# Optimization experiments

Hardware: AMD Instinct MI355X
Metric: run time of the kernel (lower is better)

## Reference

```python
import jax, jax.numpy as jnp
import numpy as np

GROUP_SIZE = 64  # quantization group size along in_features
RANK = 16
ALPHA = 1.0


def setup_inputs() -> dict:
    key = jax.random.key(0)
    ks = jax.random.split(key, 7)
    B, S, D_in, D_out = 4, 2048, 4096, 4096
    n_groups = D_in // GROUP_SIZE
    x = jax.random.normal(ks[0], (B, S, D_in), dtype=jnp.float32)
    qweight = jax.random.randint(ks[1], (D_out, D_in), 0, 16, dtype=jnp.int32)
    scales = jax.random.uniform(ks[2], (D_out, n_groups), dtype=jnp.float32) * 0.02
    zeros = jax.random.uniform(ks[3], (D_out, n_groups), dtype=jnp.float32) * 16.0
    lora_A = jax.random.normal(ks[4], (RANK, D_in), dtype=jnp.float32) / np.sqrt(D_in)
    lora_B = jax.random.normal(ks[5], (D_out, RANK), dtype=jnp.float32) * 0.01
    bias = jax.random.normal(ks[6], (D_out,), dtype=jnp.float32) * 0.02
    return {"x": x, "qweight": qweight, "scales": scales, "zeros": zeros,
            "lora_A": lora_A, "lora_B": lora_B, "bias": bias}


def _dequant(qweight, scales, zeros):
    # qweight: [O, I] int codes in [0,16); scales/zeros: [O, G] with G = I // GROUP_SIZE
    O, I = qweight.shape
    G = I // GROUP_SIZE
    q = qweight.astype(scales.dtype).reshape(O, G, GROUP_SIZE)
    w = (q - zeros[:, :, None]) * scales[:, :, None]
    return w.reshape(O, I)


def reference(x, qweight, scales, zeros, lora_A, lora_B, bias):
    # Base 4-bit dequantized matmul: y = x @ W^T
    W = _dequant(qweight, scales, zeros)            # [O, I]
    y = jnp.einsum('bsi,oi->bso', x, W)             # [B, S, O]
    # LoRA low-rank update: (alpha / rank) * (x @ A^T) @ B^T
    scaling = ALPHA / RANK
    lora = jnp.einsum('bsr,or->bso', jnp.einsum('bsi,ri->bsr', x, lora_A), lora_B)
    return y + scaling * lora + bias
```

## Files before the change

### kernel.cpp

```cpp
#include <hip/hip_runtime.h>
#include <stdint.h>
#include <stddef.h>

#define GM 8192
#define GN 4096
#define GK 4096
#define NGRP 64

typedef __bf16 bf16;
typedef __attribute__((ext_vector_type(8))) __bf16 bf16x8;
typedef __attribute__((ext_vector_type(4))) __bf16 bf16x4;
typedef __attribute__((ext_vector_type(4))) float floatx4;
typedef __attribute__((ext_vector_type(4))) int   intx4;
typedef __attribute__((ext_vector_type(8))) unsigned short ushortx8;
typedef __attribute__((ext_vector_type(4))) unsigned short ushortx4;

__device__ inline unsigned short f2bf(float f) {
  unsigned int u = __builtin_bit_cast(unsigned int, f);
  u += 0x7FFFu + ((u >> 16) & 1u);
  return (unsigned short)(u >> 16);
}
__device__ inline bf16x8 pack8(floatx4 a, floatx4 b) {
  ushortx8 u;
  u[0]=f2bf(a[0]); u[1]=f2bf(a[1]); u[2]=f2bf(a[2]); u[3]=f2bf(a[3]);
  u[4]=f2bf(b[0]); u[5]=f2bf(b[1]); u[6]=f2bf(b[2]); u[7]=f2bf(b[3]);
  return __builtin_bit_cast(bf16x8, u);
}
__device__ inline bf16x4 pack4(floatx4 a) {
  ushortx4 u;
  u[0]=f2bf(a[0]); u[1]=f2bf(a[1]); u[2]=f2bf(a[2]); u[3]=f2bf(a[3]);
  return __builtin_bit_cast(bf16x4, u);
}
__device__ inline void gll16(const void* g, void* l) {
  __builtin_amdgcn_global_load_lds(
      (const __attribute__((address_space(1))) void*)g,
      (__attribute__((address_space(3))) void*)l, 16, 0, 0);
}

__global__ __launch_bounds__(256) void qlora_prep(
    const float* __restrict__ x, bf16* __restrict__ xbf,
    const int* __restrict__ qw, const float* __restrict__ scales,
    const float* __restrict__ zeros, const float* __restrict__ lA,
    const float* __restrict__ lB, bf16* __restrict__ wbf) {
  __shared__ __align__(16) float Al[16 * 256];
  __shared__ __align__(16) float Bl[32 * 16];
  const int tid = threadIdx.x;

  if (blockIdx.x >= 2048) {
    int xb = blockIdx.x - 2048;
    #pragma unroll
    for (int t = 0; t < 4; ++t) {
      int fc = xb * 1024 + t * 256 + tid;
      int m  = fc >> 9;
      int rc = fc & 511;
      int p  = (rc & 7) ^ (m & 7);
      const float* src = x + ((size_t)fc << 3);
      floatx4 a = *(const floatx4*)src;
      floatx4 b = *(const floatx4*)(src + 4);
      *(bf16x8*)(xbf + (size_t)m * GK + ((rc >> 3) << 6) + (p << 3)) = pack8(a, b);
    }
    return;
  }

  const int n0  = (blockIdx.x & 127) * 32;
  const int kc0 = (blockIdx.x >> 7) * 256;
  #pragma unroll
  for (int t = 0; t < 4; ++t) {
    int idx = tid + t * 256;
    int r = idx >> 6, c = idx & 63;
    *(floatx4*)&Al[r * 256 + c * 4] = *(const floatx4*)&lA[(size_t)r * GK + kc0 + c * 4];
  }
  if (tid < 128) {
    int r = tid >> 2, c = tid & 3;
    *(floatx4*)&Bl[r * 16 + c * 4] = *(const floatx4*)&lB[(size_t)(n0 + r) * 16 + c * 4];
  }
  __syncthreads();

  const int klane = tid & 63;
  const int wv    = tid >> 6;
  const int k  = klane * 4;
  const int kg = kc0 + k;
  const int kb = kg & ~63;
  const int g  = kg >> 6;
  for (int it = 0; it < 8; ++it) {
    int nl = wv * 8 + it;
    int n  = n0 + nl;
    float Bv[16];
    #pragma unroll
    for (int r = 0; r < 16; ++r) Bv[r] = Bl[nl * 16 + r];
    floatx4 lacc = {0.f, 0.f, 0.f, 0.f};
    #pragma unroll
    for (int r = 0; r < 16; ++r) {
      floatx4 av = *(const floatx4*)&Al[r * 256 + k];
      lacc += av * Bv[r];
    }
    intx4 qv = *(const intx4*)&qw[(size_t)n * GK + kg];
    float s = scales[n * NGRP + g];
    float z = zeros[n * NGRP + g];
    floatx4 w;
    w[0] = ((float)qv[0] - z) * s + 0.0625f * lacc[0];
    w[1] = ((float)qv[1] - z) * s + 0.0625f * lacc[1];
    w[2] = ((float)qv[2] - z) * s + 0.0625f * lacc[2];
    w[3] = ((float)qv[3] - z) * s + 0.0625f * lacc[3];
    int p = (((kg >> 3) & 7) ^ (n & 7)) << 3;
    *(bf16x4*)&wbf[(size_t)n * GK + kb + p + (kg & 7)] = pack4(w);
  }
}

__global__ __launch_bounds__(512, 2) void qlora_gemm_pre(
    const bf16* __restrict__ Abf, const bf16* __restrict__ Wbf,
    const float* __restrict__ bias, float* __restrict__ out) {
  __shared__ __align__(16) bf16 As[2][256 * 64];
  __shared__ __align__(16) bf16 Bs[2][256 * 64];
  const int tid  = threadIdx.x;
  const int wave = tid >> 6;
  const int lane = tid & 63;
  const int wr   = wave >> 2;
  const int wc   = wave & 3;

  const int flat = blockIdx.x;
  const int xcd  = flat & 7;
  const int j    = flat >> 3;
  const int m0   = (j >> 1) * 256;
  const int n0   = (xcd * 2 + (j & 1)) * 256;

  const int srow = tid >> 3;
  const int schk = tid & 7;
  const bf16* gA = Abf + (size_t)(m0 + srow) * GK + schk * 8;
  const bf16* gB = Wbf + (size_t)(n0 + srow) * GK + schk * 8;
  char* lA = (char*)&As[0][0] + srow * 128 + schk * 16;
  char* lB = (char*)&Bs[0][0] + srow * 128 + schk * 16;

  auto stageA = [&](int buf, int tk, int half) {
    #pragma unroll
    for (int r = 0; r < 2; ++r) {
      int rb = half * 128 + r * 64;
      gll16(gA + (size_t)rb * GK + tk * 64, lA + buf * 32768 + rb * 128);
    }
  };
  auto stageB = [&](int buf, int tk, int half) {
    #pragma unroll
    for (int r = 0; r < 2; ++r) {
      int rb = half * 128 + r * 64;
      gll16(gB + (size_t)rb * GK + tk * 64, lB + buf * 32768 + rb * 128);
    }
  };

  const int rs   = lane & 7;
  const int hi   = lane >> 4;
  const int rofs = (lane & 15) * 64;
  const int c0   = ((0 + hi) ^ rs) << 3;
  const int c1   = ((4 + hi) ^ rs) << 3;
  const int arow = wr * 64;
  const int brow = wc * 32;

  bf16x8 af[4][2];
  bf16x8 bv[2][2];
  floatx4 acc[8][4] = {};

#define DSLOAD_A(P, MH) { \
    const bf16* Ap_ = &As[P][(MH * 128 + arow) * 64 + rofs]; \
    _Pragma("unroll") \
    for (int mi = 0; mi < 4; ++mi) { \
      af[mi][0] = *(const bf16x8*)(Ap_ + mi * 16 * 64 + c0); \
      af[mi][1] = *(const bf16x8*)(Ap_ + mi * 16 * 64 + c1); \
    } }
#define DSLOAD_B(P, NH) { \
    const bf16* Bp_ = &Bs[P][(NH * 128 + brow) * 64 + rofs]; \
    _Pragma("unroll") \
    for (int ni = 0; ni < 2; ++ni) { \
      bv[ni][0] = *(const bf16x8*)(Bp_ + ni * 16 * 64 + c0); \
      bv[ni][1] = *(const bf16x8*)(Bp_ + ni * 16 * 64 + c1); \
    } }
#define MFMA_PH(MH, NH) { \
    _Pragma("unroll") \
    for (int kk = 0; kk < 2; ++kk) \
      _Pragma("unroll") \
      for (int mi = 0; mi < 4; ++mi) \
        _Pragma("unroll") \
        for (int ni = 0; ni < 2; ++ni) \
          acc[MH * 4 + mi][NH * 2 + ni] = __builtin_amdgcn_mfma_f32_16x16x32_bf16( \
              af[mi][kk], bv[ni][kk], acc[MH * 4 + mi][NH * 2 + ni], 0, 0, 0); \
  }
#define BAR() __builtin_amdgcn_s_barrier()
#define LGKM0() asm volatile("s_waitcnt lgkmcnt(0)" ::: "memory")
#define PRIO(N) __builtin_amdgcn_s_setprio(N)

  stageA(0, 0, 0); stageA(0, 0, 1); stageB(0, 0, 0); stageB(0, 0, 1);
  stageA(1, 1, 0); stageB(1, 1, 1); stageA(1, 1, 1);
  asm volatile("s_waitcnt vmcnt(6)" ::: "memory");
  BAR();

  for (int t = 0; t < 64; ++t) {
    const int p = t & 1;
    DSLOAD_A(p, 0); DSLOAD_B(p, 0);
    if (t < 63) stageB(1 - p, t + 1, 0);
    BAR(); LGKM0();
    PRIO(1); MFMA_PH(0, 0); PRIO(0);
    BAR();
    DSLOAD_B(p, 1);
    if (t < 62) stageA(p, t + 2, 0);
    BAR(); LGKM0();
    PRIO(1); MFMA_PH(0, 1); PRIO(0);
    BAR();
    DSLOAD_A(p, 1);
    if (t < 62) stageB(p, t + 2, 1);
    BAR(); LGKM0();
    PRIO(1); MFMA_PH(1, 1); PRIO(0);
    BAR();
    DSLOAD_B(p, 0);
    if (t < 62) {
      stageA(p, t + 2, 1);
      asm volatile("s_waitcnt vmcnt(6)" ::: "memory");
    } else {
      asm volatile("s_waitcnt vmcnt(0)" ::: "memory");
    }
    BAR(); LGKM0();
    PRIO(1); MFMA_PH(1, 0); PRIO(0);
    BAR();
  }

#undef DSLOAD_A
#undef DSLOAD_B
#undef MFMA_PH
#undef BAR
#undef LGKM0
#undef PRIO

  const int quad = lane >> 4;
  const int col  = lane & 15;
  #pragma unroll
  for (int nh = 0; nh < 2; ++nh)
    #pragma unroll
    for (int ni = 0; ni < 2; ++ni) {
      const int gn = n0 + nh * 128 + wc * 32 + ni * 16 + col;
      const float bvv = bias[gn];
      #pragma unroll
      for (int mh = 0; mh < 2; ++mh)
        #pragma unroll
        for (int mi = 0; mi < 4; ++mi) {
          const int gm = m0 + mh * 128 + wr * 64 + mi * 16 + quad * 4;
          floatx4 a = acc[mh * 4 + mi][nh * 2 + ni];
          #pragma unroll
          for (int r = 0; r < 4; ++r)
            out[(size_t)(gm + r) * GN + gn] = a[r] + bvv;
        }
    }
}

__global__ void qlora_gemm_fb(const float* __restrict__ x, const int* __restrict__ qw,
                              const float* __restrict__ scales, const float* __restrict__ zeros,
                              const float* __restrict__ bias, float* __restrict__ out) {
  __shared__ __align__(16) bf16 As[128 * 64];
  __shared__ __align__(16) bf16 Bs[128 * 64];
  const int tid  = threadIdx.x;
  const int wave = tid >> 6;
  const int lane = tid & 63;
  const int m0 = blockIdx.x * 128;
  const int n0 = blockIdx.y * 128;
  const int wm = (wave >> 1) * 64;
  const int wn = (wave & 1) * 64;
  const int rsw = lane & 7;
  floatx4 acc[4][4] = {};
  for (int k0 = 0; k0 < GK; k0 += 64) {
    int row = tid >> 1, kh = (tid & 1) * 32;
    {
      const float* gx = x + (size_t)(m0 + row) * GK + k0 + kh;
      #pragma unroll
      for (int jj = 0; jj < 4; ++jj) {
        floatx4 a = *(const floatx4*)(gx + jj * 8);
        floatx4 b = *(const floatx4*)(gx + jj * 8 + 4);
        int p = (((kh >> 3) + jj) ^ (row & 7)) << 3;
        *(bf16x8*)&As[row * 64 + p] = pack8(a, b);
      }
    }
    {
      int n = n0 + row;
      int g = k0 >> 6;
      float s = scales[n * NGRP + g];
      float z = zeros[n * NGRP + g];
      const int* gq = qw + (size_t)n * GK + k0 + kh;
      #pragma unroll
      for (int jj = 0; jj < 4; ++jj) {
        intx4 q0 = *(const intx4*)(gq + jj * 8);
        intx4 q1 = *(const intx4*)(gq + jj * 8 + 4);
        floatx4 a, b;
        a[0]=((float)q0[0]-z)*s; a[1]=((float)q0[1]-z)*s; a[2]=((float)q0[2]-z)*s; a[3]=((float)q0[3]-z)*s;
        b[0]=((float)q1[0]-z)*s; b[1]=((float)q1[1]-z)*s; b[2]=((float)q1[2]-z)*s; b[3]=((float)q1[3]-z)*s;
        int p = (((kh >> 3) + jj) ^ (row & 7)) << 3;
        *(bf16x8*)&Bs[row * 64 + p] = pack8(a, b);
      }
    }
    __syncthreads();
    #pragma unroll
    for (int kk = 0; kk < 64; kk += 32) {
      const int cbase = kk >> 3;
      bf16x8 af[4], bfr[4];
      #pragma unroll
      for (int i = 0; i < 4; ++i)
        af[i] = *(const bf16x8*)&As[(wm + i * 16 + (lane & 15)) * 64
                                    + (((cbase + (lane >> 4)) ^ rsw) << 3)];
      #pragma unroll
      for (int i = 0; i < 4; ++i)
        bfr[i] = *(const bf16x8*)&Bs[(wn + i * 16 + (lane & 15)) * 64
                                     + (((cbase + (lane >> 4)) ^ rsw) << 3)];
      #pragma unroll
      for (int mi = 0; mi < 4; ++mi)
        #pragma unroll
        for (int ni = 0; ni < 4; ++ni)
          acc[mi][ni] = __builtin_amdgcn_mfma_f32_16x16x32_bf16(af[mi], bfr[ni], acc[mi][ni], 0, 0, 0);
    }
    __syncthreads();
  }
  const int quad = lane >> 4;
  const int col  = lane & 15;
  #pragma unroll
  for (int ni = 0; ni < 4; ++ni) {
    int gn = n0 + wn + ni * 16 + col;
    float bv = bias[gn];
    #pragma unroll
    for (int mi = 0; mi < 4; ++mi) {
      int gm = m0 + wm + mi * 16 + quad * 4;
      #pragma unroll
      for (int r = 0; r < 4; ++r)
        out[(size_t)(gm + r) * GN + gn] = acc[mi][ni][r] + bv;
    }
  }
}

extern "C" void kernel_launch(void* const* d_in, const int* in_sizes, int n_in,
                              void* d_out, int out_size, void* d_ws, size_t ws_size,
                              hipStream_t stream) {
  (void)in_sizes; (void)n_in; (void)out_size;
  const float* x      = (const float*)d_in[0];
  const int*   qw     = (const int*)d_in[1];
  const float* scales = (const float*)d_in[2];
  const float* zeros  = (const float*)d_in[3];
  const float* lA     = (const float*)d_in[4];
  const float* lB     = (const float*)d_in[5];
  const float* bias   = (const float*)d_in[6];
  float* out = (float*)d_out;

  const size_t xbf_bytes = (size_t)GM * GK * sizeof(bf16);
  const size_t wbf_bytes = (size_t)GN * GK * sizeof(bf16);
  char* ws = (char*)d_ws;

  if (ws_size >= xbf_bytes + wbf_bytes) {
    bf16* xbf = (bf16*)ws;
    bf16* wbf = (bf16*)(ws + xbf_bytes);
    qlora_prep<<<dim3(2048 + 4096), 256, 0, stream>>>(x, xbf, qw, scales, zeros, lA, lB, wbf);
    qlora_gemm_pre<<<dim3((GM / 256) * (GN / 256)), 512, 0, stream>>>(xbf, wbf, bias, out);
  } else {
    qlora_gemm_fb<<<dim3(GM / 128, GN / 128), 256, 0, stream>>>(x, qw, scales, zeros, bias, out);
  }
}
```

Baseline: 536.5 us.

## Double-buffer LDS fragment registers in GEMM loop and hoist LoRA A loads in prep

The main GEMM loop now keeps two register sets for A and B fragments. The next phase's LDS reads are issued before the current phase's MFMAs, and the explicit lgkmcnt(0) waits are gone, so shared-memory latency can overlap with matrix math. Launch bounds drop to one block per CU to make room for the extra VGPRs. LDS use already allows only one block per CU, so no real occupancy is lost. The dequant/prep kernel now loads each lora_A row vector once and accumulates all 8 output rows together, instead of reloading it per row, at the cost of more live registers.

```diff
diff --git a/kernel.cpp b/kernel.cpp
--- a/kernel.cpp
+++ b/kernel.cpp
@@ -82,32 +82,33 @@
   const int kg = kc0 + k;
   const int kb = kg & ~63;
   const int g  = kg >> 6;
+
+  floatx4 lacc[8] = {};
+  #pragma unroll
+  for (int r = 0; r < 16; ++r) {
+    floatx4 av = *(const floatx4*)&Al[r * 256 + k];
+    #pragma unroll
+    for (int it = 0; it < 8; ++it)
+      lacc[it] += av * Bl[(wv * 8 + it) * 16 + r];
+  }
+
+  #pragma unroll
   for (int it = 0; it < 8; ++it) {
-    int nl = wv * 8 + it;
-    int n  = n0 + nl;
-    float Bv[16];
-    #pragma unroll
-    for (int r = 0; r < 16; ++r) Bv[r] = Bl[nl * 16 + r];
-    floatx4 lacc = {0.f, 0.f, 0.f, 0.f};
-    #pragma unroll
-    for (int r = 0; r < 16; ++r) {
-      floatx4 av = *(const floatx4*)&Al[r * 256 + k];
-      lacc += av * Bv[r];
-    }
+    int n  = n0 + wv * 8 + it;
     intx4 qv = *(const intx4*)&qw[(size_t)n * GK + kg];
     float s = scales[n * NGRP + g];
     float z = zeros[n * NGRP + g];
     floatx4 w;
-    w[0] = ((float)qv[0] - z) * s + 0.0625f * lacc[0];
-    w[1] = ((float)qv[1] - z) * s + 0.0625f * lacc[1];
-    w[2] = ((float)qv[2] - z) * s + 0.0625f * lacc[2];
-    w[3] = ((float)qv[3] - z) * s + 0.0625f * lacc[3];
+    w[0] = ((float)qv[0] - z) * s + 0.0625f * lacc[it][0];
+    w[1] = ((float)qv[1] - z) * s + 0.0625f * lacc[it][1];
+    w[2] = ((float)qv[2] - z) * s + 0.0625f * lacc[it][2];
+    w[3] = ((float)qv[3] - z) * s + 0.0625f * lacc[it][3];
     int p = (((kg >> 3) & 7) ^ (n & 7)) << 3;
     *(bf16x4*)&wbf[(size_t)n * GK + kb + p + (kg & 7)] = pack4(w);
   }
 }
 
-__global__ __launch_bounds__(512, 2) void qlora_gemm_pre(
+__global__ __launch_bounds__(512, 1) void qlora_gemm_pre(
     const bf16* __restrict__ Abf, const bf16* __restrict__ Wbf,
     const float* __restrict__ bias, float* __restrict__ out) {
   __shared__ __align__(16) bf16 As[2][256 * 64];
@@ -154,25 +155,24 @@
   const int arow = wr * 64;
   const int brow = wc * 32;
 
-  bf16x8 af[4][2];
-  bf16x8 bv[2][2];
+  bf16x8 a0[4][2], a1[4][2], b0[2][2], b1[2][2];
   floatx4 acc[8][4] = {};
 
-#define DSLOAD_A(P, MH) { \
+#define RD_A(DST, P, MH) { \
     const bf16* Ap_ = &As[P][(MH * 128 + arow) * 64 + rofs]; \
     _Pragma("unroll") \
     for (int mi = 0; mi < 4; ++mi) { \
-      af[mi][0] = *(const bf16x8*)(Ap_ + mi * 16 * 64 + c0); \
-      af[mi][1] = *(const bf16x8*)(Ap_ + mi * 16 * 64 + c1); \
+      DST[mi][0] = *(const bf16x8*)(Ap_ + mi * 16 * 64 + c0); \
+      DST[mi][1] = *(const bf16x8*)(Ap_ + mi * 16 * 64 + c1); \
     } }
-#define DSLOAD_B(P, NH) { \
+#define RD_B(DST, P, NH) { \
     const bf16* Bp_ = &Bs[P][(NH * 128 + brow) * 64 + rofs]; \
     _Pragma("unroll") \
     for (int ni = 0; ni < 2; ++ni) { \
-      bv[ni][0] = *(const bf16x8*)(Bp_ + ni * 16 * 64 + c0); \
-      bv[ni][1] = *(const bf16x8*)(Bp_ + ni * 16 * 64 + c1); \
+      DST[ni][0] = *(const bf16x8*)(Bp_ + ni * 16 * 64 + c0); \
+      DST[ni][1] = *(const bf16x8*)(Bp_ + ni * 16 * 64 + c1); \
     } }
-#define MFMA_PH(MH, NH) { \
+#define MFMA_PH(MH, NH, AR, BR) { \
     _Pragma("unroll") \
     for (int kk = 0; kk < 2; ++kk) \
       _Pragma("unroll") \
@@ -180,51 +180,51 @@
         _Pragma("unroll") \
         for (int ni = 0; ni < 2; ++ni) \
           acc[MH * 4 + mi][NH * 2 + ni] = __builtin_amdgcn_mfma_f32_16x16x32_bf16( \
-              af[mi][kk], bv[ni][kk], acc[MH * 4 + mi][NH * 2 + ni], 0, 0, 0); \
+              AR[mi][kk], BR[ni][kk], acc[MH * 4 + mi][NH * 2 + ni], 0, 0, 0); \
   }
 #define BAR() __builtin_amdgcn_s_barrier()
-#define LGKM0() asm volatile("s_waitcnt lgkmcnt(0)" ::: "memory")
 #define PRIO(N) __builtin_amdgcn_s_setprio(N)
 
   stageA(0, 0, 0); stageA(0, 0, 1); stageB(0, 0, 0); stageB(0, 0, 1);
   stageA(1, 1, 0); stageB(1, 1, 1); stageA(1, 1, 1);
   asm volatile("s_waitcnt vmcnt(6)" ::: "memory");
   BAR();
+  RD_A(a0, 0, 0); RD_B(b0, 0, 0);
 
   for (int t = 0; t < 64; ++t) {
     const int p = t & 1;
-    DSLOAD_A(p, 0); DSLOAD_B(p, 0);
     if (t < 63) stageB(1 - p, t + 1, 0);
-    BAR(); LGKM0();
-    PRIO(1); MFMA_PH(0, 0); PRIO(0);
-    BAR();
-    DSLOAD_B(p, 1);
+    BAR();
+    RD_B(b1, p, 1);
+    PRIO(1); MFMA_PH(0, 0, a0, b0); PRIO(0);
+    BAR();
     if (t < 62) stageA(p, t + 2, 0);
-    BAR(); LGKM0();
-    PRIO(1); MFMA_PH(0, 1); PRIO(0);
-    BAR();
-    DSLOAD_A(p, 1);
+    BAR();
+    RD_A(a1, p, 1);
+    PRIO(1); MFMA_PH(0, 1, a0, b1); PRIO(0);
+    BAR();
     if (t < 62) stageB(p, t + 2, 1);
-    BAR(); LGKM0();
-    PRIO(1); MFMA_PH(1, 1); PRIO(0);
-    BAR();
-    DSLOAD_B(p, 0);
+    BAR();
+    RD_B(b0, p, 0);
+    PRIO(1); MFMA_PH(1, 1, a1, b1); PRIO(0);
+    BAR();
     if (t < 62) {
       stageA(p, t + 2, 1);
       asm volatile("s_waitcnt vmcnt(6)" ::: "memory");
     } else {
       asm volatile("s_waitcnt vmcnt(0)" ::: "memory");
     }
-    BAR(); LGKM0();
-    PRIO(1); MFMA_PH(1, 0); PRIO(0);
-    BAR();
-  }
-
-#undef DSLOAD_A
-#undef DSLOAD_B
+    BAR();
+    if (t < 63) { RD_A(a0, 1 - p, 0); }
+    PRIO(1); MFMA_PH(1, 0, a1, b0); PRIO(0);
+    if (t < 63) { RD_B(b0, 1 - p, 0); }
+    BAR();
+  }
+
+#undef RD_A
+#undef RD_B
 #undef MFMA_PH
 #undef BAR
-#undef LGKM0
 #undef PRIO
 
   const int quad = lane >> 4;
```

Result: slower. 578.8 us (+7.9%).
